# Kernel optimization log

Measured on AMD Instinct MI355X. Metric: run time of the kernel, lower is better.

The kernel has to match this reference:

```python
import jax, jax.numpy as jnp
import numpy as np

L, B, S, H, NH, F = 4, 2, 1024, 1024, 16, 4096
DH = H // NH

def setup_inputs() -> dict:
    key = jax.random.key(0)
    ks = jax.random.split(key, 16)
    std = 0.02
    return {
        'x': jax.random.normal(ks[0], (B, S, H), jnp.float32),
        'attention_mask': jnp.ones((B, S, S), jnp.float32),
        'wq': jax.random.normal(ks[1], (L, H, H), jnp.float32) * std,
        'bq': jnp.zeros((L, H), jnp.float32),
        'wk': jax.random.normal(ks[2], (L, H, H), jnp.float32) * std,
        'bk': jnp.zeros((L, H), jnp.float32),
        'wv': jax.random.normal(ks[3], (L, H, H), jnp.float32) * std,
        'bv': jnp.zeros((L, H), jnp.float32),
        'wo_attn': jax.random.normal(ks[4], (L, H, H), jnp.float32) * std,
        'bo_attn': jnp.zeros((L, H), jnp.float32),
        'alpha_attn': jax.random.uniform(ks[5], (L,), jnp.float32) * 0.1,
        'wi': jax.random.normal(ks[6], (L, H, F), jnp.float32) * std,
        'bi': jnp.zeros((L, F), jnp.float32),
        'wo_ffn': jax.random.normal(ks[7], (L, F, H), jnp.float32) * std,
        'bo_ffn': jnp.zeros((L, H), jnp.float32),
        'alpha_ffn': jax.random.uniform(ks[8], (L,), jnp.float32) * 0.1,
    }

def _heads(t):
    # [B,S,H] -> [B,NH,S,DH]
    return t.reshape(B, S, NH, DH).transpose(0, 2, 1, 3)

def reference(x, attention_mask, wq, bq, wk, bk, wv, bv, wo_attn, bo_attn,
              alpha_attn, wi, bi, wo_ffn, bo_ffn, alpha_ffn):
    # additive mask: (1 - mask) * -10000, broadcast over heads
    adder = (1.0 - attention_mask)[:, None, :, :] * -10000.0  # [B,1,S,S]
    scale = 1.0 / jnp.sqrt(jnp.asarray(DH, x.dtype))
    for l in range(L):
        q = _heads(x @ wq[l] + bq[l])
        k = _heads(x @ wk[l] + bk[l])
        v = _heads(x @ wv[l] + bv[l])
        scores = jnp.einsum('bhqd,bhkd->bhqk', q, k) * scale + adder
        probs = jax.nn.softmax(scores, axis=-1)
        ctx = jnp.einsum('bhqk,bhkd->bhqd', probs, v)
        ctx = ctx.transpose(0, 2, 1, 3).reshape(B, S, H)
        attn_out = ctx @ wo_attn[l] + bo_attn[l]
        x = x + alpha_attn[l] * attn_out  # rezero residual
        inter = jax.nn.gelu(x @ wi[l] + bi[l], approximate=True)
        ffn_out = inter @ wo_ffn[l] + bo_ffn[l]
        x = x + alpha_ffn[l] * ffn_out  # rezero residual
    return x
```

## Files before the change

kernel.cpp:

```cpp
#include <hip/hip_runtime.h>
#include <cstdint>

#define B_  2
#define S_  1024
#define H_  1024
#define NH_ 16
#define DH_ 64
#define F_  4096
#define L_  4
#define M_  (B_*S_)

typedef __bf16 bf16;
typedef __bf16 bf16x8 __attribute__((ext_vector_type(8)));
typedef __bf16 bf16x4 __attribute__((ext_vector_type(4)));
typedef __bf16 bf16x2 __attribute__((ext_vector_type(2)));
typedef float  f32x4  __attribute__((ext_vector_type(4)));

__device__ __forceinline__ void async_ld16(void* lds, const void* g) {
  auto* lp = reinterpret_cast<__attribute__((address_space(3))) unsigned int*>(
      reinterpret_cast<uintptr_t>(lds));
  const auto* gp = reinterpret_cast<const __attribute__((address_space(1))) unsigned int*>(
      reinterpret_cast<uintptr_t>(g));
  __builtin_amdgcn_global_load_lds(gp, lp, 16, 0, 0);
}

__device__ __forceinline__ float gelu_tanh(float x) {
  float u = 0.7978845608028654f * (x + 0.044715f * x * x * x);
  u = fminf(fmaxf(u, -15.f), 15.f);
  float e = __builtin_amdgcn_exp2f(u * 2.8853900817779268f);
  return 0.5f * x * (1.f + (e - 1.f) / (e + 1.f));
}

__global__ __launch_bounds__(256) void transpose_all(
    const float* __restrict__ wq, const float* __restrict__ wk,
    const float* __restrict__ wv, const float* __restrict__ wo,
    const float* __restrict__ wi, const float* __restrict__ wf,
    bf16* __restrict__ WtQKV, bf16* __restrict__ WtO,
    bf16* __restrict__ WtI, bf16* __restrict__ WtF) {
  const size_t HH = (size_t)H_ * H_;
  const size_t HF = (size_t)H_ * F_;
  int idx = blockIdx.x;
  const float* src;
  bf16* dst;
  int N, k0, n0;
  if (idx < 16384) {
    const int s = idx >> 12; idx &= 4095;
    const int l = idx >> 10; idx &= 1023;
    n0 = (idx & 31) * 32; k0 = (idx >> 5) * 32;
    N = H_;
    src = (s == 0 ? wq : s == 1 ? wk : s == 2 ? wv : wo) + (size_t)l * HH;
    dst = (s < 3) ? (WtQKV + (size_t)l * 3 * HH + (size_t)s * HH)
                  : (WtO + (size_t)l * HH);
  } else if (idx < 32768) {
    idx -= 16384;
    const int l = idx >> 12; idx &= 4095;
    n0 = (idx & 127) * 32; k0 = (idx >> 7) * 32;
    N = F_;
    src = wi + (size_t)l * HF;
    dst = WtI + (size_t)l * HF;
  } else {
    idx -= 32768;
    const int l = idx >> 12; idx &= 4095;
    n0 = (idx & 31) * 32; k0 = (idx >> 5) * 32;
    N = H_;
    src = wf + (size_t)l * HF;
    dst = WtF + (size_t)l * HF;
  }
  const int K = (N == H_ && src >= wf && src < wf + (size_t)L_ * HF) ? F_ : H_;
  __shared__ float t[32][33];
  const int x = threadIdx.x, y = threadIdx.y;
  #pragma unroll
  for (int i = 0; i < 32; i += 8)
    t[y + i][x] = src[(size_t)(k0 + y + i) * N + n0 + x];
  __syncthreads();
  #pragma unroll
  for (int i = 0; i < 32; i += 8)
    dst[(size_t)(n0 + y + i) * K + k0 + x] = (bf16)t[x][y + i];
}

__global__ __launch_bounds__(256) void prep_kernel(
    const float4* __restrict__ mask, bf16x4* __restrict__ madd,
    const float4* __restrict__ x, float4* __restrict__ xf,
    bf16x4* __restrict__ xb) {
  const int blk = blockIdx.x;
  if (blk < 2048) {
    const int i = blk * 256 + (int)threadIdx.x;
    const float c2 = -10000.f * 1.44269504088896f;
    float4 v = mask[i];
    bf16x4 o;
    o[0] = (bf16)((1.f - v.x) * c2);
    o[1] = (bf16)((1.f - v.y) * c2);
    o[2] = (bf16)((1.f - v.z) * c2);
    o[3] = (bf16)((1.f - v.w) * c2);
    madd[i] = o;
  } else {
    const int i = (blk - 2048) * 256 + (int)threadIdx.x;
    float4 v = x[i];
    xf[i] = v;
    bf16x4 b;
    b[0] = (bf16)v.x; b[1] = (bf16)v.y; b[2] = (bf16)v.z; b[3] = (bf16)v.w;
    xb[i] = b;
  }
}

__device__ __forceinline__ void gemm_core(
    const bf16* __restrict__ A, const bf16* __restrict__ Bt, int ld, int kLen,
    int m0, int n0, bf16* As, bf16* Bs, f32x4 (&acc)[4][4]) {
  const int tid = (int)threadIdx.x;
  const int w = tid >> 6, l = tid & 63;
  const int lr = l & 15, lg = l >> 4;
  const int wm = w >> 1, wn = w & 1;
  const int srow = l >> 2;
  const int scol = (l & 3) * 8;

  const bf16* ag = A  + (size_t)(m0 + w * 32 + srow) * ld + scol;
  const bf16* bg = Bt + (size_t)(n0 + w * 32 + srow) * ld + scol;
  const int soff = (w * 32) * 32;

  auto stage = [&](int buf, int kk) {
    bf16* ad = As + buf * 4096 + soff;
    bf16* bd = Bs + buf * 4096 + soff;
    async_ld16(ad,           ag + kk);
    async_ld16(ad + 16 * 32, ag + kk + (size_t)16 * ld);
    async_ld16(bd,           bg + kk);
    async_ld16(bd + 16 * 32, bg + kk + (size_t)16 * ld);
  };

  stage(0, 0);
  __syncthreads();
  int cur = 0;
  for (int k0 = 0; k0 < kLen; k0 += 32) {
    if (k0 + 32 < kLen) stage(cur ^ 1, k0 + 32);
    const bf16* Ab = As + cur * 4096;
    const bf16* Bb = Bs + cur * 4096;
    bf16x8 af[4], bv[4];
    #pragma unroll
    for (int i = 0; i < 4; ++i)
      af[i] = *(const bf16x8*)(Ab + (wm * 64 + i * 16 + lr) * 32 + lg * 8);
    #pragma unroll
    for (int i = 0; i < 4; ++i)
      bv[i] = *(const bf16x8*)(Bb + (wn * 64 + i * 16 + lr) * 32 + lg * 8);
    #pragma unroll
    for (int i = 0; i < 4; ++i)
      #pragma unroll
      for (int j = 0; j < 4; ++j)
        acc[i][j] = __builtin_amdgcn_mfma_f32_16x16x32_bf16(af[i], bv[j], acc[i][j], 0, 0, 0);
    __syncthreads();
    cur ^= 1;
  }
}

template <int MODE>
__global__ __launch_bounds__(256) void gemm128_kernel(
    const bf16* __restrict__ A, const bf16* __restrict__ Bt,
    const float* __restrict__ bias, bf16* __restrict__ outb,
    float* __restrict__ part, int N, int K, int kSlice) {
  __shared__ __align__(16) bf16 As[2 * 128 * 32];
  __shared__ __align__(16) bf16 Bs[2 * 128 * 32];
  const int m0 = blockIdx.y * 128, n0 = blockIdx.x * 128;
  const int z = blockIdx.z;
  const f32x4 z4 = {0.f, 0.f, 0.f, 0.f};
  f32x4 acc[4][4];
  #pragma unroll
  for (int i = 0; i < 4; ++i)
    #pragma unroll
    for (int j = 0; j < 4; ++j) acc[i][j] = z4;

  gemm_core(A + (size_t)z * kSlice, Bt + (size_t)z * kSlice, K, kSlice,
            m0, n0, As, Bs, acc);

  const int tid = (int)threadIdx.x;
  const int w = tid >> 6, l = tid & 63;
  const int lr = l & 15, lg = l >> 4;
  const int wm = w >> 1, wn = w & 1;
  const size_t pbase = (MODE == 3) ? (size_t)z * M_ * (size_t)N : 0;
  #pragma unroll
  for (int i = 0; i < 4; ++i) {
    const int row0 = m0 + wm * 64 + i * 16 + lg * 4;
    #pragma unroll
    for (int j = 0; j < 4; ++j) {
      const int col = n0 + wn * 64 + j * 16 + lr;
      const float bvx = (MODE == 3) ? 0.f : bias[col];
      #pragma unroll
      for (int r = 0; r < 4; ++r) {
        const size_t idx = (size_t)(row0 + r) * N + col;
        float v = acc[i][j][r] + bvx;
        if (MODE == 3) {
          part[pbase + idx] = v;
        } else {
          outb[idx] = (bf16)gelu_tanh(v);
        }
      }
    }
  }
}

__global__ __launch_bounds__(256) void reduce_residual(
    const float4* __restrict__ part, const float* __restrict__ bias,
    const float* __restrict__ alphap, float4* __restrict__ xf,
    bf16x4* __restrict__ xb) {
  const int i = blockIdx.x * 256 + (int)threadIdx.x;
  const int nper = M_ * H_ / 4;
  float4 s = part[i];
  #pragma unroll
  for (int zz = 1; zz < 4; ++zz) {
    float4 p = part[i + (size_t)zz * nper];
    s.x += p.x; s.y += p.y; s.z += p.z; s.w += p.w;
  }
  const int col = (i * 4) & (H_ - 1);
  const float4 b4 = *(const float4*)(bias + col);
  const float a = *alphap;
  float4 xv = xf[i];
  xv.x += a * (s.x + b4.x);
  xv.y += a * (s.y + b4.y);
  xv.z += a * (s.z + b4.z);
  xv.w += a * (s.w + b4.w);
  xf[i] = xv;
  bf16x4 bb;
  bb[0] = (bf16)xv.x; bb[1] = (bf16)xv.y; bb[2] = (bf16)xv.z; bb[3] = (bf16)xv.w;
  xb[i] = bb;
}

__global__ __launch_bounds__(256) void gemm_qkv64(
    const bf16* __restrict__ A, const bf16* __restrict__ Wt,
    const float* __restrict__ bq, const float* __restrict__ bk,
    const float* __restrict__ bvv,
    bf16* __restrict__ qo, bf16* __restrict__ ko, bf16* __restrict__ vt) {
  __shared__ __align__(16) bf16 As[2 * 128 * 32];
  __shared__ __align__(16) bf16 Bs[2 * 64 * 32];
  const int tid = (int)threadIdx.x;
  const int w = tid >> 6, l = tid & 63;
  const int lr = l & 15, lg = l >> 4;
  const int wm = w >> 1, wn = w & 1;
  const int srow = l >> 2, scol = (l & 3) * 8;
  const int m0 = blockIdx.y * 128, n0 = blockIdx.x * 64;

  const bf16* ag = A  + (size_t)(m0 + w * 32 + srow) * H_ + scol;
  const bf16* bg = Wt + (size_t)(n0 + w * 16 + srow) * H_ + scol;
  const int aoff = (w * 32) * 32;
  const int boff = (w * 16) * 32;

  auto stage = [&](int buf, int kk) {
    bf16* ad = As + buf * 4096 + aoff;
    bf16* bd = Bs + buf * 2048 + boff;
    async_ld16(ad,           ag + kk);
    async_ld16(ad + 16 * 32, ag + kk + (size_t)16 * H_);
    async_ld16(bd,           bg + kk);
  };

  const f32x4 z4 = {0.f, 0.f, 0.f, 0.f};
  f32x4 acc[4][2];
  #pragma unroll
  for (int i = 0; i < 4; ++i)
    #pragma unroll
    for (int j = 0; j < 2; ++j) acc[i][j] = z4;

  stage(0, 0);
  __syncthreads();
  int cur = 0;
  for (int k0 = 0; k0 < H_; k0 += 32) {
    if (k0 + 32 < H_) stage(cur ^ 1, k0 + 32);
    const bf16* Ab = As + cur * 4096;
    const bf16* Bb = Bs + cur * 2048;
    bf16x8 af[4], bv[2];
    #pragma unroll
    for (int i = 0; i < 4; ++i)
      af[i] = *(const bf16x8*)(Ab + (wm * 64 + i * 16 + lr) * 32 + lg * 8);
    #pragma unroll
    for (int j = 0; j < 2; ++j)
      bv[j] = *(const bf16x8*)(Bb + (wn * 32 + j * 16 + lr) * 32 + lg * 8);
    #pragma unroll
    for (int i = 0; i < 4; ++i)
      #pragma unroll
      for (int j = 0; j < 2; ++j)
        acc[i][j] = __builtin_amdgcn_mfma_f32_16x16x32_bf16(af[i], bv[j], acc[i][j], 0, 0, 0);
    __syncthreads();
    cur ^= 1;
  }

  if (n0 < 2048) {
    bf16* out = (n0 < 1024) ? qo : ko;
    const float* bias = (n0 < 1024) ? bq : bk;
    const int nl = n0 & 1023;
    #pragma unroll
    for (int i = 0; i < 4; ++i) {
      const int row0 = m0 + wm * 64 + i * 16 + lg * 4;
      #pragma unroll
      for (int j = 0; j < 2; ++j) {
        const int col = nl + wn * 32 + j * 16 + lr;
        const float bvx = bias[col];
        #pragma unroll
        for (int r = 0; r < 4; ++r)
          out[(size_t)(row0 + r) * H_ + col] = (bf16)(acc[i][j][r] + bvx);
      }
    }
  } else {
    const int hh = (n0 >> 6) - 32;
    #pragma unroll
    for (int i = 0; i < 4; ++i) {
      const int row0 = m0 + wm * 64 + i * 16 + lg * 4;
      const int bb = row0 >> 10, ss = row0 & (S_ - 1);
      #pragma unroll
      for (int j = 0; j < 2; ++j) {
        const int dd = wn * 32 + j * 16 + lr;
        const float bvx = bvv[hh * 64 + dd];
        bf16x4 pk;
        #pragma unroll
        for (int r = 0; r < 4; ++r) pk[r] = (bf16)(acc[i][j][r] + bvx);
        *(bf16x4*)(vt + (((size_t)(bb * NH_ + hh) * DH_ + dd) << 10) + ss) = pk;
      }
    }
  }
}

__global__ __launch_bounds__(256) void attn_kernel7(
    const bf16* __restrict__ Q, const bf16* __restrict__ Kb,
    const bf16* __restrict__ Vt, const bf16* __restrict__ madd,
    bf16* __restrict__ Ctx) {
  const int tid = (int)threadIdx.x;
  const int w = tid >> 6, l = tid & 63;
  const int lr = l & 15, lg = l >> 4;
  const int r7 = lr & 7;
  const int h = blockIdx.y, b = blockIdx.z;
  const int q0 = blockIdx.x * 64 + w * 16;

  __shared__ __align__(16) bf16 Kt[2][64 * 64];
  __shared__ __align__(16) bf16 Vs[2][64 * 64];
  __shared__ unsigned int Pu[4][16][36];

  const bf16* qp = Q + ((size_t)(b * S_ + q0 + lr)) * H_ + h * DH_;
  const bf16x8 qa0 = *(const bf16x8*)(qp + lg * 8);
  const bf16x8 qa1 = *(const bf16x8*)(qp + 32 + lg * 8);

  const f32x4 z4 = {0.f, 0.f, 0.f, 0.f};
  f32x4 acc[4];
  #pragma unroll
  for (int dt = 0; dt < 4; ++dt) acc[dt] = z4;
  float mrow = -1e30f, ssum = 0.f;

  const bf16* Kbase = Kb + ((size_t)b * S_) * H_ + h * DH_;
  const bf16* Vbase = Vt + ((size_t)(b * NH_ + h)) * DH_ * S_;
  const bf16* Mb = madd + ((size_t)(b * S_ + q0 + lr)) * S_;

  const float c1 = 0.125f * 1.44269504088896f;
  const float THR = 10.f;

  const int sub = l >> 3;
  const int cs  = ((l & 7) ^ sub) * 8;
  auto stage = [&](int buf, int kv) {
    #pragma unroll
    for (int j = 0; j < 2; ++j) {
      const int rbase = w * 16 + j * 8;
      async_ld16(&Kt[buf][rbase * 64],
                 Kbase + (size_t)(kv + rbase + sub) * H_ + cs);
      async_ld16(&Vs[buf][rbase * 64],
                 Vbase + (size_t)(rbase + sub) * S_ + kv + cs);
    }
  };

  stage(0, 0);
  bf16x4 mk[4];
  #pragma unroll
  for (int t = 0; t < 4; ++t) mk[t] = *(const bf16x4*)(Mb + t * 16 + lg * 4);
  __syncthreads();
  int cur = 0;
  #pragma unroll 1
  for (int it = 0; it < 16; ++it) {
    const int kv0 = it * 64;
    if (it < 15) stage(cur ^ 1, kv0 + 64);
    bf16x4 mkn[4];
    if (it < 15) {
      #pragma unroll
      for (int t = 0; t < 4; ++t)
        mkn[t] = *(const bf16x4*)(Mb + kv0 + 64 + t * 16 + lg * 4);
    }
    const bf16* Kc = &Kt[cur][0];
    const bf16* Vc = &Vs[cur][0];
    bf16x8 kf0[4], kf1[4];
    #pragma unroll
    for (int t = 0; t < 4; ++t) {
      kf0[t] = *(const bf16x8*)(Kc + (t * 16 + lr) * 64 + ((lg ^ r7) * 8));
      kf1[t] = *(const bf16x8*)(Kc + (t * 16 + lr) * 64 + (((4 + lg) ^ r7) * 8));
    }
    f32x4 st[4];
    __builtin_amdgcn_s_setprio(1);
    #pragma unroll
    for (int t = 0; t < 4; ++t) {
      f32x4 s = __builtin_amdgcn_mfma_f32_16x16x32_bf16(kf0[t], qa0, z4, 0, 0, 0);
      st[t] = __builtin_amdgcn_mfma_f32_16x16x32_bf16(kf1[t], qa1, s, 0, 0, 0);
    }
    __builtin_amdgcn_s_setprio(0);
    float sv[4][4];
    #pragma unroll
    for (int t = 0; t < 4; ++t)
      #pragma unroll
      for (int r = 0; r < 4; ++r)
        sv[t][r] = st[t][r] * c1 + (float)mk[t][r];
    float nm = sv[0][0];
    #pragma unroll
    for (int t = 0; t < 4; ++t)
      #pragma unroll
      for (int r = 0; r < 4; ++r) nm = fmaxf(nm, sv[t][r]);
    nm = fmaxf(nm, __shfl_xor(nm, 16));
    nm = fmaxf(nm, __shfl_xor(nm, 32));
    if (__any(nm > mrow + THR)) {
      float newm = fmaxf(mrow, nm);
      float f = __builtin_amdgcn_exp2f(mrow - newm);
      mrow = newm;
      ssum *= f;
      #pragma unroll
      for (int dt = 0; dt < 4; ++dt)
        #pragma unroll
        for (int r = 0; r < 4; ++r) acc[dt][r] *= f;
    }
    float p[4][4];
    float ps = 0.f;
    #pragma unroll
    for (int t = 0; t < 4; ++t)
      #pragma unroll
      for (int r = 0; r < 4; ++r) {
        p[t][r] = __builtin_amdgcn_exp2f(sv[t][r] - mrow);
        ps += p[t][r];
      }
    ps += __shfl_xor(ps, 16);
    ps += __shfl_xor(ps, 32);
    ssum += ps;
    #pragma unroll
    for (int t = 0; t < 4; ++t)
      #pragma unroll
      for (int hh = 0; hh < 2; ++hh) {
        union { bf16x2 v; unsigned int u; } pk;
        pk.v[0] = (bf16)p[t][2 * hh];
        pk.v[1] = (bf16)p[t][2 * hh + 1];
        Pu[w][lr][8 * t + 2 * lg + hh] = pk.u;
      }
    const bf16x8 pf0 = *(const bf16x8*)&Pu[w][lr][4 * lg];
    const bf16x8 pf1 = *(const bf16x8*)&Pu[w][lr][16 + 4 * lg];
    __builtin_amdgcn_s_setprio(1);
    #pragma unroll
    for (int dt = 0; dt < 4; ++dt) {
      bf16x8 vb0 = *(const bf16x8*)(Vc + (dt * 16 + lr) * 64 + ((lg ^ r7) * 8));
      acc[dt] = __builtin_amdgcn_mfma_f32_16x16x32_bf16(vb0, pf0, acc[dt], 0, 0, 0);
    }
    #pragma unroll
    for (int dt = 0; dt < 4; ++dt) {
      bf16x8 vb1 = *(const bf16x8*)(Vc + (dt * 16 + lr) * 64 + (((4 + lg) ^ r7) * 8));
      acc[dt] = __builtin_amdgcn_mfma_f32_16x16x32_bf16(vb1, pf1, acc[dt], 0, 0, 0);
    }
    __builtin_amdgcn_s_setprio(0);
    if (it < 15) {
      #pragma unroll
      for (int t = 0; t < 4; ++t) mk[t] = mkn[t];
    }
    __syncthreads();
    cur ^= 1;
  }
  const float inv = 1.f / ssum;
  bf16* cp = Ctx + ((size_t)(b * S_ + q0 + lr)) * H_ + h * DH_;
  #pragma unroll
  for (int dt = 0; dt < 4; ++dt) {
    bf16x4 o;
    #pragma unroll
    for (int r = 0; r < 4; ++r) o[r] = (bf16)(acc[dt][r] * inv);
    *(bf16x4*)(cp + dt * 16 + lg * 4) = o;
  }
}

extern "C" void kernel_launch(void* const* d_in, const int* in_sizes, int n_in,
                              void* d_out, int out_size, void* d_ws, size_t ws_size,
                              hipStream_t stream) {
  (void)in_sizes; (void)n_in; (void)out_size; (void)ws_size;
  const float* x    = (const float*)d_in[0];
  const float* mask = (const float*)d_in[1];
  const float* wq   = (const float*)d_in[2];
  const float* bq   = (const float*)d_in[3];
  const float* wk   = (const float*)d_in[4];
  const float* bk   = (const float*)d_in[5];
  const float* wv   = (const float*)d_in[6];
  const float* bv   = (const float*)d_in[7];
  const float* wo   = (const float*)d_in[8];
  const float* bo   = (const float*)d_in[9];
  const float* aat  = (const float*)d_in[10];
  const float* wi   = (const float*)d_in[11];
  const float* bi   = (const float*)d_in[12];
  const float* wf   = (const float*)d_in[13];
  const float* bf_  = (const float*)d_in[14];
  const float* afn  = (const float*)d_in[15];

  char* ws = (char*)d_ws;
  size_t o = 0;
  bf16* WtQKV = (bf16*)(ws + o); o += (size_t)L_ * 3 * H_ * H_ * 2;
  bf16* WtO = (bf16*)(ws + o); o += (size_t)L_ * H_ * H_ * 2;
  bf16* WtI = (bf16*)(ws + o); o += (size_t)L_ * H_ * F_ * 2;
  bf16* WtF = (bf16*)(ws + o); o += (size_t)L_ * F_ * H_ * 2;
  bf16* madd = (bf16*)(ws + o); o += (size_t)B_ * S_ * S_ * 2;
  bf16* xb  = (bf16*)(ws + o); o += (size_t)M_ * H_ * 2;
  bf16* qb  = (bf16*)(ws + o); o += (size_t)M_ * H_ * 2;
  bf16* kbf = (bf16*)(ws + o); o += (size_t)M_ * H_ * 2;
  bf16* vt  = (bf16*)(ws + o); o += (size_t)M_ * H_ * 2;
  bf16* ctx = (bf16*)(ws + o); o += (size_t)M_ * H_ * 2;
  bf16* itm = (bf16*)(ws + o); o += (size_t)M_ * F_ * 2;
  float* part = (float*)(ws + o); o += (size_t)4 * M_ * H_ * 4;

  float* xf = (float*)d_out;

  const size_t HH = (size_t)H_ * H_;
  transpose_all<<<dim3(49152), dim3(32, 8), 0, stream>>>(
      wq, wk, wv, wo, wi, wf, WtQKV, WtO, WtI, WtF);
  prep_kernel<<<dim3(4096), 256, 0, stream>>>(
      (const float4*)mask, (bf16x4*)madd, (const float4*)x, (float4*)xf,
      (bf16x4*)xb);

  for (int l = 0; l < L_; ++l) {
    gemm_qkv64<<<dim3(48, M_/128), 256, 0, stream>>>(
        xb, WtQKV + (size_t)l * 3 * HH,
        bq + l * H_, bk + l * H_, bv + l * H_, qb, kbf, vt);
    attn_kernel7<<<dim3(S_/64, NH_, B_), 256, 0, stream>>>(
        qb, kbf, vt, madd, ctx);
    gemm128_kernel<3><<<dim3(H_/128, M_/128, 4), 256, 0, stream>>>(
        ctx, WtO + (size_t)l * HH, nullptr, nullptr, part, H_, H_, H_ / 4);
    reduce_residual<<<dim3((M_ * H_ / 4) / 256), 256, 0, stream>>>(
        (const float4*)part, bo + l * H_, aat + l, (float4*)xf, (bf16x4*)xb);
    gemm128_kernel<1><<<dim3(F_/128, M_/128), 256, 0, stream>>>(
        xb, WtI + (size_t)l * H_ * F_, bi + l * F_, itm, nullptr, F_, H_, H_);
    gemm128_kernel<3><<<dim3(H_/128, M_/128, 4), 256, 0, stream>>>(
        itm, WtF + (size_t)l * F_ * H_, nullptr, nullptr, part, H_, F_, F_ / 4);
    reduce_residual<<<dim3((M_ * H_ / 4) / 256), 256, 0, stream>>>(
        (const float4*)part, bf_ + l * H_, afn + l, (float4*)xf, (bf16x4*)xb);
  }
}
```

Measured before the change: 631.7 us.

## Store split-K partials in bf16 and use 64x64 vectorized weight transpose tiles

The split-K GEMM partial sums are now written as bf16 instead of fp32, which halves the write and read traffic between the output-projection/FFN-down GEMMs and the residual reduction. The weight transpose kernel now uses 64x64 tiles with float2 loads and bf16x2 stores, so it launches a quarter as many blocks and issues wider memory accesses. The cost is precision: each partial is rounded to bf16 before summation, which adds error to the residual update. The new transpose also writes shared memory with a stride-2 column pattern that may cause bank conflicts.

```diff
diff --git a/kernel.cpp b/kernel.cpp
--- a/kernel.cpp
+++ b/kernel.cpp
@@ -42,40 +42,49 @@
   int idx = blockIdx.x;
   const float* src;
   bf16* dst;
-  int N, k0, n0;
-  if (idx < 16384) {
-    const int s = idx >> 12; idx &= 4095;
-    const int l = idx >> 10; idx &= 1023;
-    n0 = (idx & 31) * 32; k0 = (idx >> 5) * 32;
-    N = H_;
+  int N, K, k0, n0;
+  if (idx < 4096) {
+    const int s = idx >> 10;
+    const int l = (idx >> 8) & 3;
+    const int t = idx & 255;
+    n0 = (t & 15) * 64; k0 = (t >> 4) * 64;
+    N = H_; K = H_;
     src = (s == 0 ? wq : s == 1 ? wk : s == 2 ? wv : wo) + (size_t)l * HH;
     dst = (s < 3) ? (WtQKV + (size_t)l * 3 * HH + (size_t)s * HH)
                   : (WtO + (size_t)l * HH);
-  } else if (idx < 32768) {
-    idx -= 16384;
-    const int l = idx >> 12; idx &= 4095;
-    n0 = (idx & 127) * 32; k0 = (idx >> 7) * 32;
-    N = F_;
+  } else if (idx < 8192) {
+    const int j = idx - 4096;
+    const int l = j >> 10;
+    const int t = j & 1023;
+    n0 = (t & 63) * 64; k0 = (t >> 6) * 64;
+    N = F_; K = H_;
     src = wi + (size_t)l * HF;
     dst = WtI + (size_t)l * HF;
   } else {
-    idx -= 32768;
-    const int l = idx >> 12; idx &= 4095;
-    n0 = (idx & 31) * 32; k0 = (idx >> 5) * 32;
-    N = H_;
+    const int j = idx - 8192;
+    const int l = j >> 10;
+    const int t = j & 1023;
+    n0 = (t & 15) * 64; k0 = (t >> 4) * 64;
+    N = H_; K = F_;
     src = wf + (size_t)l * HF;
     dst = WtF + (size_t)l * HF;
   }
-  const int K = (N == H_ && src >= wf && src < wf + (size_t)L_ * HF) ? F_ : H_;
-  __shared__ float t[32][33];
+  __shared__ float t[64][65];
   const int x = threadIdx.x, y = threadIdx.y;
   #pragma unroll
-  for (int i = 0; i < 32; i += 8)
-    t[y + i][x] = src[(size_t)(k0 + y + i) * N + n0 + x];
+  for (int i = 0; i < 64; i += 8) {
+    const float2 v = *(const float2*)(src + (size_t)(k0 + y + i) * N + n0 + 2 * x);
+    t[2 * x][y + i] = v.x;
+    t[2 * x + 1][y + i] = v.y;
+  }
   __syncthreads();
   #pragma unroll
-  for (int i = 0; i < 32; i += 8)
-    dst[(size_t)(n0 + y + i) * K + k0 + x] = (bf16)t[x][y + i];
+  for (int i = 0; i < 64; i += 8) {
+    bf16x2 o;
+    o[0] = (bf16)t[y + i][2 * x];
+    o[1] = (bf16)t[y + i][2 * x + 1];
+    *(bf16x2*)(dst + (size_t)(n0 + y + i) * K + k0 + 2 * x) = o;
+  }
 }
 
 __global__ __launch_bounds__(256) void prep_kernel(
@@ -154,7 +163,7 @@
 __global__ __launch_bounds__(256) void gemm128_kernel(
     const bf16* __restrict__ A, const bf16* __restrict__ Bt,
     const float* __restrict__ bias, bf16* __restrict__ outb,
-    float* __restrict__ part, int N, int K, int kSlice) {
+    int N, int K, int kSlice) {
   __shared__ __align__(16) bf16 As[2 * 128 * 32];
   __shared__ __align__(16) bf16 Bs[2 * 128 * 32];
   const int m0 = blockIdx.y * 128, n0 = blockIdx.x * 128;
@@ -186,7 +195,7 @@
         const size_t idx = (size_t)(row0 + r) * N + col;
         float v = acc[i][j][r] + bvx;
         if (MODE == 3) {
-          part[pbase + idx] = v;
+          outb[pbase + idx] = (bf16)v;
         } else {
           outb[idx] = (bf16)gelu_tanh(v);
         }
@@ -196,25 +205,26 @@
 }
 
 __global__ __launch_bounds__(256) void reduce_residual(
-    const float4* __restrict__ part, const float* __restrict__ bias,
+    const bf16x4* __restrict__ part, const float* __restrict__ bias,
     const float* __restrict__ alphap, float4* __restrict__ xf,
     bf16x4* __restrict__ xb) {
   const int i = blockIdx.x * 256 + (int)threadIdx.x;
   const int nper = M_ * H_ / 4;
-  float4 s = part[i];
-  #pragma unroll
-  for (int zz = 1; zz < 4; ++zz) {
-    float4 p = part[i + (size_t)zz * nper];
-    s.x += p.x; s.y += p.y; s.z += p.z; s.w += p.w;
+  float s[4] = {0.f, 0.f, 0.f, 0.f};
+  #pragma unroll
+  for (int zz = 0; zz < 4; ++zz) {
+    const bf16x4 p = part[i + (size_t)zz * nper];
+    #pragma unroll
+    for (int k = 0; k < 4; ++k) s[k] += (float)p[k];
   }
   const int col = (i * 4) & (H_ - 1);
   const float4 b4 = *(const float4*)(bias + col);
   const float a = *alphap;
   float4 xv = xf[i];
-  xv.x += a * (s.x + b4.x);
-  xv.y += a * (s.y + b4.y);
-  xv.z += a * (s.z + b4.z);
-  xv.w += a * (s.w + b4.w);
+  xv.x += a * (s[0] + b4.x);
+  xv.y += a * (s[1] + b4.y);
+  xv.z += a * (s[2] + b4.z);
+  xv.w += a * (s[3] + b4.w);
   xf[i] = xv;
   bf16x4 bb;
   bb[0] = (bf16)xv.x; bb[1] = (bf16)xv.y; bb[2] = (bf16)xv.z; bb[3] = (bf16)xv.w;
@@ -500,12 +510,12 @@
   bf16* vt  = (bf16*)(ws + o); o += (size_t)M_ * H_ * 2;
   bf16* ctx = (bf16*)(ws + o); o += (size_t)M_ * H_ * 2;
   bf16* itm = (bf16*)(ws + o); o += (size_t)M_ * F_ * 2;
-  float* part = (float*)(ws + o); o += (size_t)4 * M_ * H_ * 4;
+  bf16* partb = (bf16*)(ws + o); o += (size_t)4 * M_ * H_ * 2;
 
   float* xf = (float*)d_out;
 
   const size_t HH = (size_t)H_ * H_;
-  transpose_all<<<dim3(49152), dim3(32, 8), 0, stream>>>(
+  transpose_all<<<dim3(12288), dim3(32, 8), 0, stream>>>(
       wq, wk, wv, wo, wi, wf, WtQKV, WtO, WtI, WtF);
   prep_kernel<<<dim3(4096), 256, 0, stream>>>(
       (const float4*)mask, (bf16x4*)madd, (const float4*)x, (float4*)xf,
@@ -518,14 +528,14 @@
     attn_kernel7<<<dim3(S_/64, NH_, B_), 256, 0, stream>>>(
         qb, kbf, vt, madd, ctx);
     gemm128_kernel<3><<<dim3(H_/128, M_/128, 4), 256, 0, stream>>>(
-        ctx, WtO + (size_t)l * HH, nullptr, nullptr, part, H_, H_, H_ / 4);
+        ctx, WtO + (size_t)l * HH, nullptr, partb, H_, H_, H_ / 4);
     reduce_residual<<<dim3((M_ * H_ / 4) / 256), 256, 0, stream>>>(
-        (const float4*)part, bo + l * H_, aat + l, (float4*)xf, (bf16x4*)xb);
+        (const bf16x4*)partb, bo + l * H_, aat + l, (float4*)xf, (bf16x4*)xb);
     gemm128_kernel<1><<<dim3(F_/128, M_/128), 256, 0, stream>>>(
-        xb, WtI + (size_t)l * H_ * F_, bi + l * F_, itm, nullptr, F_, H_, H_);
+        xb, WtI + (size_t)l * H_ * F_, bi + l * F_, itm, F_, H_, H_);
     gemm128_kernel<3><<<dim3(H_/128, M_/128, 4), 256, 0, stream>>>(
-        itm, WtF + (size_t)l * F_ * H_, nullptr, nullptr, part, H_, F_, F_ / 4);
+        itm, WtF + (size_t)l * F_ * H_, nullptr, partb, H_, F_, F_ / 4);
     reduce_residual<<<dim3((M_ * H_ / 4) / 256), 256, 0, stream>>>(
-        (const float4*)part, bf_ + l * H_, afn + l, (float4*)xf, (bf16x4*)xb);
-  }
-}
+        (const bf16x4*)partb, bf_ + l * H_, afn + l, (float4*)xf, (bf16x4*)xb);
+  }
+}
```

After: 606.5 us. 1.04x faster.
